# Optimization experiments

Measured on AMD Instinct MI355X. Metric: run time of the kernel, lower is better.

Reference implementation:

```python
import jax, jax.numpy as jnp
import numpy as np

N = 100000
E = 1600000
IN_C, HID, HEADS, OUT_C = 128, 32, 4, 32
NEG_SLOPE = 0.2


def gat_layer(x, edge_index, W, att_src, att_dst, bias, concat):
    """PyG-style GATConv: h = xW, per-edge attention, segment softmax over dst, scatter-add."""
    n = x.shape[0]
    H, C = att_src.shape
    h = (x @ W).reshape(n, H, C)                      # [N, H, C]
    src, dst = edge_index[0], edge_index[1]
    a_s = jnp.sum(h * att_src, axis=-1)               # [N, H]
    a_d = jnp.sum(h * att_dst, axis=-1)               # [N, H]
    e = jax.nn.leaky_relu(a_s[src] + a_d[dst], NEG_SLOPE)   # [E, H]
    # numerically stable segment softmax over incoming edges of each dst node
    m = jax.ops.segment_max(e, dst, num_segments=n)   # [N, H]
    ex = jnp.exp(e - m[dst])
    denom = jax.ops.segment_sum(ex, dst, num_segments=n)
    alpha = ex / denom[dst]                           # [E, H]
    msg = h[src] * alpha[:, :, None]                  # [E, H, C]
    out = jax.ops.segment_sum(msg, dst, num_segments=n)  # [N, H, C]
    out = out.reshape(n, H * C) if concat else out.mean(axis=1)
    return out + bias


def add_self_loops(edge_index, n):
    ar = jnp.arange(n, dtype=edge_index.dtype)
    loops = jnp.stack([ar, ar])
    return jnp.concatenate([edge_index, loops], axis=1)


def setup_inputs() -> dict:
    key = jax.random.key(0)
    ks = jax.random.split(key, 10)
    x = jax.random.normal(ks[0], (N, IN_C), dtype=jnp.float32)
    edge_index = jax.random.randint(ks[1], (2, E), 0, N, dtype=jnp.int64)
    s = 0.1
    W1 = jax.random.normal(ks[2], (IN_C, HEADS * HID), dtype=jnp.float32) * s
    att_src1 = jax.random.normal(ks[3], (HEADS, HID), dtype=jnp.float32) * s
    att_dst1 = jax.random.normal(ks[4], (HEADS, HID), dtype=jnp.float32) * s
    b1 = jnp.zeros((HEADS * HID,), dtype=jnp.float32)
    W2 = jax.random.normal(ks[5], (HEADS * HID, OUT_C), dtype=jnp.float32) * s
    att_src2 = jax.random.normal(ks[6], (1, OUT_C), dtype=jnp.float32) * s
    att_dst2 = jax.random.normal(ks[7], (1, OUT_C), dtype=jnp.float32) * s
    b2 = jnp.zeros((OUT_C,), dtype=jnp.float32)
    return {"x": x, "edge_index": edge_index,
            "W1": W1, "att_src1": att_src1, "att_dst1": att_dst1, "b1": b1,
            "W2": W2, "att_src2": att_src2, "att_dst2": att_dst2, "b2": b2}


def reference(x, edge_index, W1, att_src1, att_dst1, b1, W2, att_src2, att_dst2, b2):
    ei = add_self_loops(edge_index, x.shape[0])
    h = gat_layer(x, ei, W1, att_src1, att_dst1, b1, concat=True)
    h = jax.nn.elu(h)
    h = gat_layer(h, ei, W2, att_src2, att_dst2, b2, concat=False)
    return jax.nn.log_softmax(h, axis=1)
```

## Files before the change

### kernel.cpp

```cpp
#include <hip/hip_runtime.h>
#include <hip/hip_fp16.h>
#include <math.h>

#define IN_C   128
#define HEADS  4
#define F1     128
#define OUT_C  32
#define NEG    0.2f
#define SH     8
#define CHA    8192
#define SCB    4096

__device__ __forceinline__ unsigned short f2h(float f) {
    return __half_as_ushort(__float2half_rn(f));
}
__device__ __forceinline__ float h2f(unsigned short u) {
    return __half2float(__ushort_as_half(u));
}
__device__ __forceinline__ float hlo(unsigned u) { return h2f((unsigned short)(u & 0xffffu)); }
__device__ __forceinline__ float hhi(unsigned u) { return h2f((unsigned short)(u >> 16)); }
__device__ __forceinline__ unsigned pk2(float a, float b) {
    return (unsigned)f2h(a) | ((unsigned)f2h(b) << 16);
}
typedef _Float16 h2v __attribute__((ext_vector_type(2)));
__device__ __forceinline__ h2v u2h2(unsigned u) {
    h2v r; __builtin_memcpy(&r, &u, 4); return r;
}
__device__ __forceinline__ float dot2(unsigned a, unsigned b, float c) {
    return __builtin_amdgcn_fdot2(u2h2(a), u2h2(b), c, false);
}
#define PERM_LO 0x05040100u
#define PERM_HI 0x07060302u
__device__ __forceinline__ float pdot(unsigned b, unsigned a, unsigned sel, h2v pv, float c) {
    return __builtin_amdgcn_fdot2(u2h2(__builtin_amdgcn_perm(b, a, sel)), pv, c, false);
}

__global__ __launch_bounds__(256) void k_bhist(
    const int* __restrict__ ei, int* __restrict__ bmat, int E_, int n, int NB, int NC)
{
    __shared__ int h[512];
    int t = threadIdx.x, c = blockIdx.x;
    for (int i = t; i < NB; i += 256) h[i] = 0;
    __syncthreads();
    int e0 = c * CHA, e1 = min(e0 + CHA, E_ + n);
    for (int e = e0 + t; e < e1; e += 256) {
        int d = (e < E_) ? ei[E_ + e] : e - E_;
        atomicAdd(&h[d >> SH], 1);
    }
    __syncthreads();
    for (int i = t; i < NB; i += 256) bmat[i * NC + c] = h[i];
}

__global__ __launch_bounds__(256) void k_scanA(
    int* __restrict__ bmat, int* __restrict__ bsums, int M)
{
    __shared__ int sm[256];
    int t = threadIdx.x;
    int base = blockIdx.x * SCB + t * 16;
    int v[16];
    int s = 0;
    #pragma unroll
    for (int j = 0; j < 16; ++j) {
        int i = base + j;
        v[j] = (i < M) ? bmat[i] : 0;
        s += v[j];
    }
    sm[t] = s;
    __syncthreads();
    for (int off = 1; off < 256; off <<= 1) {
        int a = (t >= off) ? sm[t - off] : 0;
        __syncthreads();
        sm[t] += a;
        __syncthreads();
    }
    int excl = sm[t] - s;
    #pragma unroll
    for (int j = 0; j < 16; ++j) {
        int i = base + j;
        if (i < M) bmat[i] = excl;
        excl += v[j];
    }
    if (t == 255) bsums[blockIdx.x] = sm[255];
}

__global__ __launch_bounds__(256) void k_scanB(int* __restrict__ bsums, int NBLK)
{
    __shared__ int sm[256];
    int t = threadIdx.x;
    int v = (t < NBLK) ? bsums[t] : 0;
    sm[t] = v;
    __syncthreads();
    for (int off = 1; off < 256; off <<= 1) {
        int a = (t >= off) ? sm[t - off] : 0;
        __syncthreads();
        sm[t] += a;
        __syncthreads();
    }
    if (t < NBLK) bsums[t] = sm[t] - v;
}

__global__ __launch_bounds__(256) void k_scanC(
    int* __restrict__ bmat, const int* __restrict__ bsums, int M)
{
    int i = blockIdx.x * 256 + threadIdx.x;
    if (i < M) bmat[i] += bsums[i >> 12];
}

__global__ __launch_bounds__(256) void k_bscatter(
    const int* __restrict__ ei, const int* __restrict__ bmat,
    unsigned* __restrict__ recs, int E_, int n, int NB, int NC)
{
    __shared__ int cur[512];
    int t = threadIdx.x, c = blockIdx.x;
    for (int i = t; i < NB; i += 256) cur[i] = bmat[i * NC + c];
    __syncthreads();
    int e0 = c * CHA, e1 = min(e0 + CHA, E_ + n);
    for (int e = e0 + t; e < e1; e += 256) {
        int s, d;
        if (e < E_) { s = ei[e]; d = ei[E_ + e]; } else { s = d = e - E_; }
        int b = d >> SH;
        int p = atomicAdd(&cur[b], 1);
        recs[p] = ((unsigned)(d & ((1 << SH) - 1)) << 17) | (unsigned)s;
    }
}

__global__ __launch_bounds__(256) void k_bfill(
    const unsigned* __restrict__ recs, const int* __restrict__ bmat,
    int* __restrict__ row_off, int* __restrict__ csr, int n, int NB, int NC, int EE)
{
    __shared__ int deg[256];
    __shared__ int cur[256];
    int t = threadIdx.x, b = blockIdx.x;
    int r0 = bmat[b * NC];
    int r1 = (b + 1 < NB) ? bmat[(b + 1) * NC] : EE;
    deg[t] = 0;
    __syncthreads();
    for (int i = r0 + t; i < r1; i += 256)
        atomicAdd(&deg[recs[i] >> 17], 1);
    __syncthreads();
    int v = deg[t];
    for (int off = 1; off < 256; off <<= 1) {
        int a = (t >= off) ? deg[t - off] : 0;
        __syncthreads();
        deg[t] += a;
        __syncthreads();
    }
    int excl = deg[t] - v;
    int dst = (b << SH) + t;
    if (dst < n) row_off[dst] = r0 + excl;
    cur[t] = excl;
    if (b == NB - 1 && t == 0) row_off[n] = EE;
    __syncthreads();
    for (int i = r0 + t; i < r1; i += 256) {
        unsigned rec = recs[i];
        int dl = rec >> 17;
        int p = atomicAdd(&cur[dl], 1);
        csr[r0 + p] = (int)(rec & 0x1FFFFu);
    }
}

__global__ __launch_bounds__(256) void k_gemm1(
    const float* __restrict__ x, const float* __restrict__ W,
    const float* __restrict__ as_w, const float* __restrict__ ad_w,
    unsigned short* __restrict__ h1h, float* __restrict__ as1,
    float* __restrict__ ad1, int n)
{
    __shared__ unsigned Ws2[64 * 64];
    __shared__ unsigned xs2[64 * 64];
    int t = threadIdx.x;
    int half = blockIdx.x & 1;
    int n0 = (blockIdx.x >> 1) * 64;

    for (int i = t; i < 64 * 16; i += 256) {
        int k2 = i >> 4, c4 = (i & 15) * 4;
        const float* w0 = &W[(2 * k2) * 128 + half * 64 + c4];
        const float* w1 = &W[(2 * k2 + 1) * 128 + half * 64 + c4];
        float4 a = *(const float4*)w0;
        float4 b = *(const float4*)w1;
        uint4 p;
        p.x = pk2(a.x, b.x); p.y = pk2(a.y, b.y);
        p.z = pk2(a.z, b.z); p.w = pk2(a.w, b.w);
        *(uint4*)&Ws2[k2 * 64 + c4] = p;
    }
    for (int i = t; i < 64 * 32; i += 256) {
        int nl = i & 63, k4 = (i >> 6) * 4;
        int nn = n0 + nl;
        float4 v = (nn < n) ? *(const float4*)&x[(size_t)nn * 128 + k4]
                            : make_float4(0.f, 0.f, 0.f, 0.f);
        xs2[(k4 >> 1) * 64 + nl]       = pk2(v.x, v.y);
        xs2[((k4 >> 1) + 1) * 64 + nl] = pk2(v.z, v.w);
    }
    __syncthreads();

    int tx = t & 15, ty = t >> 4;
    float acc[4][4] = {};
    #pragma unroll 4
    for (int k2 = 0; k2 < 64; ++k2) {
        uint4 a = *(uint4*)&xs2[k2 * 64 + ty * 4];
        uint4 b = *(uint4*)&Ws2[k2 * 64 + tx * 4];
        unsigned av[4] = {a.x, a.y, a.z, a.w};
        unsigned bv[4] = {b.x, b.y, b.z, b.w};
        #pragma unroll
        for (int i = 0; i < 4; ++i)
            #pragma unroll
            for (int j = 0; j < 4; ++j)
                acc[i][j] = dot2(av[i], bv[j], acc[i][j]);
    }
    int cbase = half * 64 + tx * 4;
    float4 aws = *(const float4*)&as_w[cbase];
    float4 awd = *(const float4*)&ad_w[cbase];
    float sa[4], sd[4];
    #pragma unroll
    for (int i = 0; i < 4; ++i) {
        int nn = n0 + ty * 4 + i;
        sa[i] = acc[i][0]*aws.x + acc[i][1]*aws.y + acc[i][2]*aws.z + acc[i][3]*aws.w;
        sd[i] = acc[i][0]*awd.x + acc[i][1]*awd.y + acc[i][2]*awd.z + acc[i][3]*awd.w;
        if (nn < n) {
            ushort4 p;
            p.x = f2h(acc[i][0]); p.y = f2h(acc[i][1]);
            p.z = f2h(acc[i][2]); p.w = f2h(acc[i][3]);
            *(ushort4*)&h1h[(size_t)nn * 128 + cbase] = p;
        }
    }
    #pragma unroll
    for (int o = 1; o < 8; o <<= 1) {
        #pragma unroll
        for (int i = 0; i < 4; ++i) {
            sa[i] += __shfl_xor(sa[i], o);
            sd[i] += __shfl_xor(sd[i], o);
        }
    }
    if ((tx & 7) == 0) {
        int head = half * 2 + (tx >> 3);
        #pragma unroll
        for (int i = 0; i < 4; ++i) {
            int nn = n0 + ty * 4 + i;
            if (nn < n) {
                as1[(size_t)nn * 4 + head] = sa[i];
                ad1[(size_t)nn * 4 + head] = sd[i];
            }
        }
    }
}

__global__ __launch_bounds__(256) void k_gemm2(
    const float* __restrict__ z, const float* __restrict__ W,
    const float* __restrict__ as_w, const float* __restrict__ ad_w,
    unsigned short* __restrict__ h2h, float* __restrict__ as2,
    float* __restrict__ ad2, int n)
{
    __shared__ unsigned Ws2[64 * 32];
    __shared__ unsigned zs2[64 * 64];
    int t = threadIdx.x;
    int n0 = blockIdx.x * 64;

    for (int i = t; i < 64 * 8; i += 256) {
        int k2 = i >> 3, c4 = (i & 7) * 4;
        float4 a = *(const float4*)&W[(2 * k2) * 32 + c4];
        float4 b = *(const float4*)&W[(2 * k2 + 1) * 32 + c4];
        uint4 p;
        p.x = pk2(a.x, b.x); p.y = pk2(a.y, b.y);
        p.z = pk2(a.z, b.z); p.w = pk2(a.w, b.w);
        *(uint4*)&Ws2[k2 * 32 + c4] = p;
    }
    for (int i = t; i < 64 * 32; i += 256) {
        int nl = i & 63, k4 = (i >> 6) * 4;
        int nn = n0 + nl;
        float4 v = (nn < n) ? *(const float4*)&z[(size_t)nn * 128 + k4]
                            : make_float4(0.f, 0.f, 0.f, 0.f);
        zs2[(k4 >> 1) * 64 + nl]       = pk2(v.x, v.y);
        zs2[((k4 >> 1) + 1) * 64 + nl] = pk2(v.z, v.w);
    }
    __syncthreads();

    int tx = t & 7, ty = t >> 3;
    float acc[2][4] = {};
    #pragma unroll 4
    for (int k2 = 0; k2 < 64; ++k2) {
        uint2 a = *(uint2*)&zs2[k2 * 64 + ty * 2];
        uint4 b = *(uint4*)&Ws2[k2 * 32 + tx * 4];
        unsigned av[2] = {a.x, a.y};
        unsigned bv[4] = {b.x, b.y, b.z, b.w};
        #pragma unroll
        for (int i = 0; i < 2; ++i)
            #pragma unroll
            for (int j = 0; j < 4; ++j)
                acc[i][j] = dot2(av[i], bv[j], acc[i][j]);
    }
    float4 aws = *(const float4*)&as_w[tx * 4];
    float4 awd = *(const float4*)&ad_w[tx * 4];
    float sa[2], sd[2];
    #pragma unroll
    for (int i = 0; i < 2; ++i) {
        int nn = n0 + ty * 2 + i;
        sa[i] = acc[i][0]*aws.x + acc[i][1]*aws.y + acc[i][2]*aws.z + acc[i][3]*aws.w;
        sd[i] = acc[i][0]*awd.x + acc[i][1]*awd.y + acc[i][2]*awd.z + acc[i][3]*awd.w;
        if (nn < n) {
            ushort4 p;
            p.x = f2h(acc[i][0]); p.y = f2h(acc[i][1]);
            p.z = f2h(acc[i][2]); p.w = f2h(acc[i][3]);
            *(ushort4*)&h2h[(size_t)nn * 32 + tx * 4] = p;
        }
    }
    #pragma unroll
    for (int o = 1; o < 8; o <<= 1) {
        #pragma unroll
        for (int i = 0; i < 2; ++i) {
            sa[i] += __shfl_xor(sa[i], o);
            sd[i] += __shfl_xor(sd[i], o);
        }
    }
    if (tx == 0) {
        #pragma unroll
        for (int i = 0; i < 2; ++i) {
            int nn = n0 + ty * 2 + i;
            if (nn < n) { as2[nn] = sa[i]; ad2[nn] = sd[i]; }
        }
    }
}

__global__ __launch_bounds__(256) void k_gat1(
    const int* __restrict__ row_off, const int* __restrict__ csr,
    const float* __restrict__ as1, const float* __restrict__ ad1,
    const unsigned short* __restrict__ h1h, const float* __restrict__ b1,
    float* __restrict__ z, int n)
{
    int nb = threadIdx.x >> 4;
    int hl = threadIdx.x & 15;
    int node = blockIdx.x * 16 + nb;
    if (node >= n) return;
    __shared__ int            s_src[16][16];
    __shared__ unsigned short s_p16[16][4][16];
    int* ssrc = s_src[nb];
    unsigned short (*sp16)[16] = s_p16[nb];

    const char* h1b = (const char*)h1h;
    int chb  = hl << 4;
    int head = hl >> 2;

    float4 addv = *(const float4*)&ad1[(size_t)node * 4];
    int beg = row_off[node], end = row_off[node + 1];

    float sr0 = 0.f, sr1 = 0.f, sr2 = 0.f, sr3 = 0.f;
    float acc0 = 0.f, acc1 = 0.f, acc2 = 0.f, acc3 = 0.f;
    float acc4 = 0.f, acc5 = 0.f, acc6 = 0.f, acc7 = 0.f;

    for (int c = beg; c < end; c += 16) {
        int cnt = min(16, end - c);
        bool has = hl < cnt;
        float ls0 = 0.f, ls1 = 0.f, ls2 = 0.f, ls3 = 0.f;
        if (has) {
            int sA = csr[c + hl];
            ssrc[hl] = sA << 8;
            float4 av = *(const float4*)(as1 + ((unsigned)sA << 2));
            float v;
            v = av.x + addv.x; v = v > 0.f ? v : NEG * v; v = fminf(v, 10.f);
            unsigned short q0 = f2h(__expf(v));
            v = av.y + addv.y; v = v > 0.f ? v : NEG * v; v = fminf(v, 10.f);
            unsigned short q1 = f2h(__expf(v));
            v = av.z + addv.z; v = v > 0.f ? v : NEG * v; v = fminf(v, 10.f);
            unsigned short q2 = f2h(__expf(v));
            v = av.w + addv.w; v = v > 0.f ? v : NEG * v; v = fminf(v, 10.f);
            unsigned short q3 = f2h(__expf(v));
            sp16[0][hl] = q0; sp16[1][hl] = q1;
            sp16[2][hl] = q2; sp16[3][hl] = q3;
            ls0 = h2f(q0); ls1 = h2f(q1); ls2 = h2f(q2); ls3 = h2f(q3);
        }
        #pragma unroll
        for (int o = 8; o; o >>= 1) {
            ls0 += __shfl_xor(ls0, o);
            ls1 += __shfl_xor(ls1, o);
            ls2 += __shfl_xor(ls2, o);
            ls3 += __shfl_xor(ls3, o);
        }
        sr0 += ls0; sr1 += ls1; sr2 += ls2; sr3 += ls3;
        __threadfence_block();

        #define PAIR1(j) {                                                    \
            int2 oo = *(const int2*)&ssrc[j];                                 \
            unsigned pp = *(const unsigned*)&sp16[head][j];                   \
            uint4 A = *(const uint4*)(h1b + (unsigned)(oo.x + chb));          \
            uint4 B = *(const uint4*)(h1b + (unsigned)(oo.y + chb));          \
            h2v pv = u2h2(pp);                                                \
            acc0 = pdot(B.x, A.x, PERM_LO, pv, acc0);                         \
            acc1 = pdot(B.x, A.x, PERM_HI, pv, acc1);                         \
            acc2 = pdot(B.y, A.y, PERM_LO, pv, acc2);                         \
            acc3 = pdot(B.y, A.y, PERM_HI, pv, acc3);                         \
            acc4 = pdot(B.z, A.z, PERM_LO, pv, acc4);                         \
            acc5 = pdot(B.z, A.z, PERM_HI, pv, acc5);                         \
            acc6 = pdot(B.w, A.w, PERM_LO, pv, acc6);                         \
            acc7 = pdot(B.w, A.w, PERM_HI, pv, acc7);                         \
        }
        int jj = 0;
        for (; jj + 4 <= cnt; jj += 4) {
            PAIR1(jj);
            PAIR1(jj + 2);
        }
        if (jj + 2 <= cnt) {
            PAIR1(jj);
            jj += 2;
        }
        if (jj < cnt) {
            int o0 = ssrc[jj];
            float p = h2f(sp16[head][jj]);
            uint4 A = *(const uint4*)(h1b + (unsigned)(o0 + chb));
            acc0 = fmaf(p, hlo(A.x), acc0);
            acc1 = fmaf(p, hhi(A.x), acc1);
            acc2 = fmaf(p, hlo(A.y), acc2);
            acc3 = fmaf(p, hhi(A.y), acc3);
            acc4 = fmaf(p, hlo(A.z), acc4);
            acc5 = fmaf(p, hhi(A.z), acc5);
            acc6 = fmaf(p, hlo(A.w), acc6);
            acc7 = fmaf(p, hhi(A.w), acc7);
        }
        #undef PAIR1
    }
    float srh = head == 0 ? sr0 : head == 1 ? sr1 : head == 2 ? sr2 : sr3;
    float inv = 1.0f / srh;
    float4 bb0 = *(const float4*)&b1[hl * 8];
    float4 bb1 = *(const float4*)&b1[hl * 8 + 4];
    float v0 = acc0 * inv + bb0.x;
    float v1 = acc1 * inv + bb0.y;
    float v2 = acc2 * inv + bb0.z;
    float v3 = acc3 * inv + bb0.w;
    float v4 = acc4 * inv + bb1.x;
    float v5 = acc5 * inv + bb1.y;
    float v6 = acc6 * inv + bb1.z;
    float v7 = acc7 * inv + bb1.w;
    v0 = v0 > 0.f ? v0 : (__expf(v0) - 1.f);
    v1 = v1 > 0.f ? v1 : (__expf(v1) - 1.f);
    v2 = v2 > 0.f ? v2 : (__expf(v2) - 1.f);
    v3 = v3 > 0.f ? v3 : (__expf(v3) - 1.f);
    v4 = v4 > 0.f ? v4 : (__expf(v4) - 1.f);
    v5 = v5 > 0.f ? v5 : (__expf(v5) - 1.f);
    v6 = v6 > 0.f ? v6 : (__expf(v6) - 1.f);
    v7 = v7 > 0.f ? v7 : (__expf(v7) - 1.f);
    float* zr = &z[(size_t)node * F1 + hl * 8];
    *(float4*)zr       = make_float4(v0, v1, v2, v3);
    *(float4*)(zr + 4) = make_float4(v4, v5, v6, v7);
}

__global__ __launch_bounds__(256) void k_gat2(
    const int* __restrict__ row_off, const int* __restrict__ csr,
    const float* __restrict__ as2, const float* __restrict__ ad2,
    const unsigned short* __restrict__ h2h, const float* __restrict__ b2,
    float* __restrict__ y, int n)
{
    int nb = threadIdx.x >> 4;
    int hl = threadIdx.x & 15;
    int node = blockIdx.x * 16 + nb;
    if (node >= n) return;
    __shared__ int            s_src[16][16];
    __shared__ unsigned short s_p16[16][16];
    int* ssrc = s_src[nb];
    unsigned short* sp16 = s_p16[nb];

    const char* h2b = (const char*)h2h;
    int chb = hl << 2;

    float addv = ad2[node];
    int beg = row_off[node], end = row_off[node + 1];
    float sr = 0.f, acc0 = 0.f, acc1 = 0.f;

    for (int c = beg; c < end; c += 16) {
        int cnt = min(16, end - c);
        bool has = hl < cnt;
        float ls = 0.f;
        if (has) {
            int sA = csr[c + hl];
            ssrc[hl] = sA << 6;
            float v = as2[(unsigned)sA] + addv;
            v = v > 0.f ? v : NEG * v;
            v = fminf(v, 10.f);
            unsigned short q = f2h(__expf(v));
            sp16[hl] = q;
            ls = h2f(q);
        }
        #pragma unroll
        for (int o = 8; o; o >>= 1) ls += __shfl_xor(ls, o);
        sr += ls;
        __threadfence_block();

        #define PAIR2(j) {                                                    \
            int2 oo = *(const int2*)&ssrc[j];                                 \
            unsigned pp = *(const unsigned*)&sp16[j];                         \
            unsigned ua = *(const unsigned*)(h2b + (unsigned)(oo.x + chb));   \
            unsigned ub = *(const unsigned*)(h2b + (unsigned)(oo.y + chb));   \
            h2v pv = u2h2(pp);                                                \
            acc0 = pdot(ub, ua, PERM_LO, pv, acc0);                           \
            acc1 = pdot(ub, ua, PERM_HI, pv, acc1);                           \
        }
        int jj = 0;
        for (; jj + 4 <= cnt; jj += 4) {
            PAIR2(jj);
            PAIR2(jj + 2);
        }
        if (jj + 2 <= cnt) {
            PAIR2(jj);
            jj += 2;
        }
        if (jj < cnt) {
            unsigned ua = *(const unsigned*)(h2b + (unsigned)(ssrc[jj] + chb));
            float p = h2f(sp16[jj]);
            acc0 = fmaf(p, hlo(ua), acc0);
            acc1 = fmaf(p, hhi(ua), acc1);
        }
        #undef PAIR2
    }
    float inv = 1.0f / sr;
    float2 bb = *(const float2*)&b2[hl * 2];
    float v0 = acc0 * inv + bb.x;
    float v1 = acc1 * inv + bb.y;
    float m = fmaxf(v0, v1);
    #pragma unroll
    for (int o = 8; o; o >>= 1) m = fmaxf(m, __shfl_xor(m, o));
    float ss = __expf(v0 - m) + __expf(v1 - m);
    #pragma unroll
    for (int o = 8; o; o >>= 1) ss += __shfl_xor(ss, o);
    float lg = m + logf(ss);
    *(float2*)&y[(size_t)node * OUT_C + hl * 2] = make_float2(v0 - lg, v1 - lg);
}

extern "C" void kernel_launch(void* const* d_in, const int* in_sizes, int n_in,
                              void* d_out, int out_size, void* d_ws, size_t ws_size,
                              hipStream_t stream) {
    const float* x    = (const float*)d_in[0];
    const int*   ei   = (const int*)d_in[1];
    const float* W1   = (const float*)d_in[2];
    const float* as1w = (const float*)d_in[3];
    const float* ad1w = (const float*)d_in[4];
    const float* b1   = (const float*)d_in[5];
    const float* W2   = (const float*)d_in[6];
    const float* as2w = (const float*)d_in[7];
    const float* ad2w = (const float*)d_in[8];
    const float* b2   = (const float*)d_in[9];
    float* out = (float*)d_out;

    int n  = in_sizes[0] / IN_C;
    int E_ = in_sizes[1] / 2;
    int EE = E_ + n;

    int NB = (n + (1 << SH) - 1) >> SH;
    int NC = (EE + CHA - 1) / CHA;
    int M  = NB * NC;
    int NBLK = (M + SCB - 1) / SCB;

    char* w = (char*)d_ws;
    size_t off = 0;
    auto take = [&](size_t elems) { void* p = w + off; off += ((elems * 4 + 255) & ~(size_t)255); return p; };
    int* bmat      = (int*)take((size_t)M);
    int* bsums     = (int*)take(256);
    unsigned* recs = (unsigned*)take((size_t)EE);
    int* row_off   = (int*)take((size_t)n + 1);
    int* csr       = (int*)take((size_t)EE);
    float* as1     = (float*)take((size_t)n * 4);
    float* ad1     = (float*)take((size_t)n * 4);
    unsigned short* h1h = (unsigned short*)take((size_t)n * 64);
    float* z       = (float*)take((size_t)n * 128);
    unsigned short* h2h = (unsigned short*)take((size_t)n * 16);
    float* as2     = (float*)take((size_t)n);
    float* ad2     = (float*)take((size_t)n);

    k_bhist   <<<NC, 256, 0, stream>>>(ei, bmat, E_, n, NB, NC);
    k_scanA   <<<NBLK, 256, 0, stream>>>(bmat, bsums, M);
    k_scanB   <<<1, 256, 0, stream>>>(bsums, NBLK);
    k_scanC   <<<(M + 255) / 256, 256, 0, stream>>>(bmat, bsums, M);
    k_bscatter<<<NC, 256, 0, stream>>>(ei, bmat, recs, E_, n, NB, NC);
    k_bfill   <<<NB, 256, 0, stream>>>(recs, bmat, row_off, csr, n, NB, NC, EE);

    int nt = (n + 63) / 64;
    k_gemm1<<<nt * 2, 256, 0, stream>>>(x, W1, as1w, ad1w, h1h, as1, ad1, n);
    int gG = (n + 15) / 16;
    k_gat1<<<gG, 256, 0, stream>>>(row_off, csr, as1, ad1, h1h, b1, z, n);

    k_gemm2<<<nt, 256, 0, stream>>>(z, W2, as2w, ad2w, h2h, as2, ad2, n);
    k_gat2<<<gG, 256, 0, stream>>>(row_off, csr, as2, ad2, h2h, b2, out, n);
}
```

Measured before the change: 332.0 us.

## Sort nodes by in-degree for load-balanced GAT aggregation, widen edge chunks to 32

Builds a degree histogram during CSR construction, scans it, and scatters node ids into a degree-bucketed permutation. Both GAT aggregation kernels then process nodes in that order, so the 16-lane groups inside a block handle nodes of similar degree and diverge less. The softmax-weight stage now handles 32 edges per chunk with each lane computing two edges, which halves the outer loop trips for typical degrees. The cost is two extra small kernels and scattered output writes, because nodes are no longer processed in index order.

Result: slower. 611.0 us (+84.0%).

```diff
diff --git a/kernel.cpp b/kernel.cpp
--- a/kernel.cpp
+++ b/kernel.cpp
@@ -108,10 +108,11 @@
 
 __global__ __launch_bounds__(256) void k_bscatter(
     const int* __restrict__ ei, const int* __restrict__ bmat,
-    unsigned* __restrict__ recs, int E_, int n, int NB, int NC)
+    unsigned* __restrict__ recs, int* __restrict__ dhist, int E_, int n, int NB, int NC)
 {
     __shared__ int cur[512];
     int t = threadIdx.x, c = blockIdx.x;
+    if (c == 0 && t < 256) dhist[t] = 0;
     for (int i = t; i < NB; i += 256) cur[i] = bmat[i * NC + c];
     __syncthreads();
     int e0 = c * CHA, e1 = min(e0 + CHA, E_ + n);
@@ -126,7 +127,8 @@
 
 __global__ __launch_bounds__(256) void k_bfill(
     const unsigned* __restrict__ recs, const int* __restrict__ bmat,
-    int* __restrict__ row_off, int* __restrict__ csr, int n, int NB, int NC, int EE)
+    int* __restrict__ row_off, int* __restrict__ csr, int* __restrict__ dhist,
+    int n, int NB, int NC, int EE)
 {
     __shared__ int deg[256];
     __shared__ int cur[256];
@@ -147,7 +149,10 @@
     }
     int excl = deg[t] - v;
     int dst = (b << SH) + t;
-    if (dst < n) row_off[dst] = r0 + excl;
+    if (dst < n) {
+        row_off[dst] = r0 + excl;
+        atomicAdd(&dhist[min(v, 255)], 1);
+    }
     cur[t] = excl;
     if (b == NB - 1 && t == 0) row_off[n] = EE;
     __syncthreads();
@@ -157,6 +162,28 @@
         int p = atomicAdd(&cur[dl], 1);
         csr[r0 + p] = (int)(rec & 0x1FFFFu);
     }
+}
+
+__global__ __launch_bounds__(256) void k_pscatter(
+    const int* __restrict__ row_off, int* __restrict__ cur,
+    int* __restrict__ perm, int n)
+{
+    __shared__ int bh[256], bbase[256];
+    int t = threadIdx.x;
+    int i = blockIdx.x * 256 + t;
+    bh[t] = 0;
+    __syncthreads();
+    int bin = 0, rk = 0;
+    bool val = i < n;
+    if (val) {
+        int deg = row_off[i + 1] - row_off[i];
+        bin = min(deg, 255);
+        rk = atomicAdd(&bh[bin], 1);
+    }
+    __syncthreads();
+    if (bh[t] > 0) bbase[t] = atomicAdd(&cur[t], bh[t]);
+    __syncthreads();
+    if (val) perm[bbase[bin] + rk] = i;
 }
 
 __global__ __launch_bounds__(256) void k_gemm1(
@@ -320,6 +347,7 @@
 }
 
 __global__ __launch_bounds__(256) void k_gat1(
+    const int* __restrict__ perm,
     const int* __restrict__ row_off, const int* __restrict__ csr,
     const float* __restrict__ as1, const float* __restrict__ ad1,
     const unsigned short* __restrict__ h1h, const float* __restrict__ b1,
@@ -327,12 +355,13 @@
 {
     int nb = threadIdx.x >> 4;
     int hl = threadIdx.x & 15;
-    int node = blockIdx.x * 16 + nb;
-    if (node >= n) return;
-    __shared__ int            s_src[16][16];
-    __shared__ unsigned short s_p16[16][4][16];
+    int r = blockIdx.x * 16 + nb;
+    if (r >= n) return;
+    int node = perm[r];
+    __shared__ int            s_src[16][32];
+    __shared__ unsigned short s_p16[16][4][32];
     int* ssrc = s_src[nb];
-    unsigned short (*sp16)[16] = s_p16[nb];
+    unsigned short (*sp16)[32] = s_p16[nb];
 
     const char* h1b = (const char*)h1h;
     int chb  = hl << 4;
@@ -345,26 +374,38 @@
     float acc0 = 0.f, acc1 = 0.f, acc2 = 0.f, acc3 = 0.f;
     float acc4 = 0.f, acc5 = 0.f, acc6 = 0.f, acc7 = 0.f;
 
-    for (int c = beg; c < end; c += 16) {
-        int cnt = min(16, end - c);
-        bool has = hl < cnt;
+    for (int c = beg; c < end; c += 32) {
+        int cnt = min(32, end - c);
+        int e0 = hl << 1;
         float ls0 = 0.f, ls1 = 0.f, ls2 = 0.f, ls3 = 0.f;
-        if (has) {
-            int sA = csr[c + hl];
-            ssrc[hl] = sA << 8;
-            float4 av = *(const float4*)(as1 + ((unsigned)sA << 2));
+        if (e0 < cnt) {
+            int sA = csr[c + e0];
+            ssrc[e0] = sA << 8;
+            float4 avA = *(const float4*)(as1 + ((unsigned)sA << 2));
             float v;
-            v = av.x + addv.x; v = v > 0.f ? v : NEG * v; v = fminf(v, 10.f);
-            unsigned short q0 = f2h(__expf(v));
-            v = av.y + addv.y; v = v > 0.f ? v : NEG * v; v = fminf(v, 10.f);
-            unsigned short q1 = f2h(__expf(v));
-            v = av.z + addv.z; v = v > 0.f ? v : NEG * v; v = fminf(v, 10.f);
-            unsigned short q2 = f2h(__expf(v));
-            v = av.w + addv.w; v = v > 0.f ? v : NEG * v; v = fminf(v, 10.f);
-            unsigned short q3 = f2h(__expf(v));
-            sp16[0][hl] = q0; sp16[1][hl] = q1;
-            sp16[2][hl] = q2; sp16[3][hl] = q3;
-            ls0 = h2f(q0); ls1 = h2f(q1); ls2 = h2f(q2); ls3 = h2f(q3);
+            unsigned short qa0, qa1, qa2, qa3;
+            unsigned short qb0 = 0, qb1 = 0, qb2 = 0, qb3 = 0;
+            v = avA.x + addv.x; v = v > 0.f ? v : NEG * v; qa0 = f2h(__expf(fminf(v, 10.f)));
+            v = avA.y + addv.y; v = v > 0.f ? v : NEG * v; qa1 = f2h(__expf(fminf(v, 10.f)));
+            v = avA.z + addv.z; v = v > 0.f ? v : NEG * v; qa2 = f2h(__expf(fminf(v, 10.f)));
+            v = avA.w + addv.w; v = v > 0.f ? v : NEG * v; qa3 = f2h(__expf(fminf(v, 10.f)));
+            if (e0 + 1 < cnt) {
+                int sB = csr[c + e0 + 1];
+                ssrc[e0 + 1] = sB << 8;
+                float4 avB = *(const float4*)(as1 + ((unsigned)sB << 2));
+                v = avB.x + addv.x; v = v > 0.f ? v : NEG * v; qb0 = f2h(__expf(fminf(v, 10.f)));
+                v = avB.y + addv.y; v = v > 0.f ? v : NEG * v; qb1 = f2h(__expf(fminf(v, 10.f)));
+                v = avB.z + addv.z; v = v > 0.f ? v : NEG * v; qb2 = f2h(__expf(fminf(v, 10.f)));
+                v = avB.w + addv.w; v = v > 0.f ? v : NEG * v; qb3 = f2h(__expf(fminf(v, 10.f)));
+            }
+            *(unsigned*)&sp16[0][e0] = (unsigned)qa0 | ((unsigned)qb0 << 16);
+            *(unsigned*)&sp16[1][e0] = (unsigned)qa1 | ((unsigned)qb1 << 16);
+            *(unsigned*)&sp16[2][e0] = (unsigned)qa2 | ((unsigned)qb2 << 16);
+            *(unsigned*)&sp16[3][e0] = (unsigned)qa3 | ((unsigned)qb3 << 16);
+            ls0 = h2f(qa0) + h2f(qb0);
+            ls1 = h2f(qa1) + h2f(qb1);
+            ls2 = h2f(qa2) + h2f(qb2);
+            ls3 = h2f(qa3) + h2f(qb3);
         }
         #pragma unroll
         for (int o = 8; o; o >>= 1) {
@@ -441,6 +482,7 @@
 }
 
 __global__ __launch_bounds__(256) void k_gat2(
+    const int* __restrict__ perm,
     const int* __restrict__ row_off, const int* __restrict__ csr,
     const float* __restrict__ as2, const float* __restrict__ ad2,
     const unsigned short* __restrict__ h2h, const float* __restrict__ b2,
@@ -448,10 +490,11 @@
 {
     int nb = threadIdx.x >> 4;
     int hl = threadIdx.x & 15;
-    int node = blockIdx.x * 16 + nb;
-    if (node >= n) return;
-    __shared__ int            s_src[16][16];
-    __shared__ unsigned short s_p16[16][16];
+    int r = blockIdx.x * 16 + nb;
+    if (r >= n) return;
+    int node = perm[r];
+    __shared__ int            s_src[16][32];
+    __shared__ unsigned short s_p16[16][32];
     int* ssrc = s_src[nb];
     unsigned short* sp16 = s_p16[nb];
 
@@ -462,19 +505,26 @@
     int beg = row_off[node], end = row_off[node + 1];
     float sr = 0.f, acc0 = 0.f, acc1 = 0.f;
 
-    for (int c = beg; c < end; c += 16) {
-        int cnt = min(16, end - c);
-        bool has = hl < cnt;
+    for (int c = beg; c < end; c += 32) {
+        int cnt = min(32, end - c);
+        int e0 = hl << 1;
         float ls = 0.f;
-        if (has) {
-            int sA = csr[c + hl];
-            ssrc[hl] = sA << 6;
+        if (e0 < cnt) {
+            int sA = csr[c + e0];
+            ssrc[e0] = sA << 6;
             float v = as2[(unsigned)sA] + addv;
             v = v > 0.f ? v : NEG * v;
-            v = fminf(v, 10.f);
-            unsigned short q = f2h(__expf(v));
-            sp16[hl] = q;
-            ls = h2f(q);
+            unsigned short qa = f2h(__expf(fminf(v, 10.f)));
+            unsigned short qb = 0;
+            if (e0 + 1 < cnt) {
+                int sB = csr[c + e0 + 1];
+                ssrc[e0 + 1] = sB << 6;
+                float w = as2[(unsigned)sB] + addv;
+                w = w > 0.f ? w : NEG * w;
+                qb = f2h(__expf(fminf(w, 10.f)));
+            }
+            *(unsigned*)&sp16[e0] = (unsigned)qa | ((unsigned)qb << 16);
+            ls = h2f(qa) + h2f(qb);
         }
         #pragma unroll
         for (int o = 8; o; o >>= 1) ls += __shfl_xor(ls, o);
@@ -561,18 +611,24 @@
     float* as2     = (float*)take((size_t)n);
     float* ad2     = (float*)take((size_t)n);
 
+    int* dhist = bsums;
+    int* perm  = (int*)recs;
+
     k_bhist   <<<NC, 256, 0, stream>>>(ei, bmat, E_, n, NB, NC);
     k_scanA   <<<NBLK, 256, 0, stream>>>(bmat, bsums, M);
     k_scanB   <<<1, 256, 0, stream>>>(bsums, NBLK);
     k_scanC   <<<(M + 255) / 256, 256, 0, stream>>>(bmat, bsums, M);
-    k_bscatter<<<NC, 256, 0, stream>>>(ei, bmat, recs, E_, n, NB, NC);
-    k_bfill   <<<NB, 256, 0, stream>>>(recs, bmat, row_off, csr, n, NB, NC, EE);
+    k_bscatter<<<NC, 256, 0, stream>>>(ei, bmat, recs, dhist, E_, n, NB, NC);
+    k_bfill   <<<NB, 256, 0, stream>>>(recs, bmat, row_off, csr, dhist, n, NB, NC, EE);
+
+    k_scanB   <<<1, 256, 0, stream>>>(dhist, 256);
+    k_pscatter<<<(n + 255) / 256, 256, 0, stream>>>(row_off, dhist, perm, n);
 
     int nt = (n + 63) / 64;
     k_gemm1<<<nt * 2, 256, 0, stream>>>(x, W1, as1w, ad1w, h1h, as1, ad1, n);
     int gG = (n + 15) / 16;
-    k_gat1<<<gG, 256, 0, stream>>>(row_off, csr, as1, ad1, h1h, b1, z, n);
+    k_gat1<<<gG, 256, 0, stream>>>(perm, row_off, csr, as1, ad1, h1h, b1, z, n);
 
     k_gemm2<<<nt, 256, 0, stream>>>(z, W2, as2w, ad2w, h2h, as2, ad2, n);
-    k_gat2<<<gG, 256, 0, stream>>>(row_off, csr, as2, ad2, h2h, b2, out, n);
-}
+    k_gat2<<<gG, 256, 0, stream>>>(perm, row_off, csr, as2, ad2, h2h, b2, out, n);
+}
```

## Remap layer-2 aggregation to 4 lanes per node with 16-byte gathers

Applied to the files above, without the earlier changes.

The second GAT aggregation kernel now assigns 4 threads per destination node (64 nodes per block) instead of 16. Each lane gathers 16 bytes (8 fp16 channels) per source edge and keeps 8 accumulators, and edge chunks grow to 32 so each lane computes 8 attention weights. This cuts the number of small gather instructions and shuffle steps, and raises the number of nodes per wave so low-degree nodes waste fewer lanes. In exchange it adds register pressure and serializes more per-edge exp work onto each lane.

Measured after the change: 339.3 us. +2.2%, slower.

```diff
diff --git a/kernel.cpp b/kernel.cpp
--- a/kernel.cpp
+++ b/kernel.cpp
@@ -446,49 +446,68 @@
     const unsigned short* __restrict__ h2h, const float* __restrict__ b2,
     float* __restrict__ y, int n)
 {
-    int nb = threadIdx.x >> 4;
-    int hl = threadIdx.x & 15;
-    int node = blockIdx.x * 16 + nb;
+    int nb = threadIdx.x >> 2;
+    int hl = threadIdx.x & 3;
+    int node = blockIdx.x * 64 + nb;
     if (node >= n) return;
-    __shared__ int            s_src[16][16];
-    __shared__ unsigned short s_p16[16][16];
+    __shared__ int            s_src[64][34];
+    __shared__ unsigned short s_p16[64][34];
     int* ssrc = s_src[nb];
     unsigned short* sp16 = s_p16[nb];
 
     const char* h2b = (const char*)h2h;
-    int chb = hl << 2;
+    int chb = hl << 4;
 
     float addv = ad2[node];
     int beg = row_off[node], end = row_off[node + 1];
-    float sr = 0.f, acc0 = 0.f, acc1 = 0.f;
-
-    for (int c = beg; c < end; c += 16) {
-        int cnt = min(16, end - c);
-        bool has = hl < cnt;
+    float sr = 0.f;
+    float acc0 = 0.f, acc1 = 0.f, acc2 = 0.f, acc3 = 0.f;
+    float acc4 = 0.f, acc5 = 0.f, acc6 = 0.f, acc7 = 0.f;
+
+    for (int c = beg; c < end; c += 32) {
+        int cnt = min(32, end - c);
+        int e0 = hl << 3;
         float ls = 0.f;
-        if (has) {
-            int sA = csr[c + hl];
-            ssrc[hl] = sA << 6;
-            float v = as2[(unsigned)sA] + addv;
-            v = v > 0.f ? v : NEG * v;
-            v = fminf(v, 10.f);
-            unsigned short q = f2h(__expf(v));
-            sp16[hl] = q;
-            ls = h2f(q);
-        }
-        #pragma unroll
-        for (int o = 8; o; o >>= 1) ls += __shfl_xor(ls, o);
+        #pragma unroll
+        for (int k = 0; k < 8; k += 2) {
+            int e = e0 + k;
+            if (e < cnt) {
+                unsigned short qa, qb = 0;
+                int sA = csr[c + e];
+                ssrc[e] = sA << 6;
+                float v = as2[(unsigned)sA] + addv;
+                v = v > 0.f ? v : NEG * v;
+                qa = f2h(__expf(fminf(v, 10.f)));
+                if (e + 1 < cnt) {
+                    int sB = csr[c + e + 1];
+                    ssrc[e + 1] = sB << 6;
+                    float w2 = as2[(unsigned)sB] + addv;
+                    w2 = w2 > 0.f ? w2 : NEG * w2;
+                    qb = f2h(__expf(fminf(w2, 10.f)));
+                }
+                *(unsigned*)&sp16[e] = (unsigned)qa | ((unsigned)qb << 16);
+                ls += h2f(qa) + h2f(qb);
+            }
+        }
+        ls += __shfl_xor(ls, 1);
+        ls += __shfl_xor(ls, 2);
         sr += ls;
         __threadfence_block();
 
         #define PAIR2(j) {                                                    \
             int2 oo = *(const int2*)&ssrc[j];                                 \
             unsigned pp = *(const unsigned*)&sp16[j];                         \
-            unsigned ua = *(const unsigned*)(h2b + (unsigned)(oo.x + chb));   \
-            unsigned ub = *(const unsigned*)(h2b + (unsigned)(oo.y + chb));   \
+            uint4 A = *(const uint4*)(h2b + (unsigned)(oo.x + chb));          \
+            uint4 B = *(const uint4*)(h2b + (unsigned)(oo.y + chb));          \
             h2v pv = u2h2(pp);                                                \
-            acc0 = pdot(ub, ua, PERM_LO, pv, acc0);                           \
-            acc1 = pdot(ub, ua, PERM_HI, pv, acc1);                           \
+            acc0 = pdot(B.x, A.x, PERM_LO, pv, acc0);                         \
+            acc1 = pdot(B.x, A.x, PERM_HI, pv, acc1);                         \
+            acc2 = pdot(B.y, A.y, PERM_LO, pv, acc2);                         \
+            acc3 = pdot(B.y, A.y, PERM_HI, pv, acc3);                         \
+            acc4 = pdot(B.z, A.z, PERM_LO, pv, acc4);                         \
+            acc5 = pdot(B.z, A.z, PERM_HI, pv, acc5);                         \
+            acc6 = pdot(B.w, A.w, PERM_LO, pv, acc6);                         \
+            acc7 = pdot(B.w, A.w, PERM_HI, pv, acc7);                         \
         }
         int jj = 0;
         for (; jj + 4 <= cnt; jj += 4) {
@@ -500,25 +519,43 @@
             jj += 2;
         }
         if (jj < cnt) {
-            unsigned ua = *(const unsigned*)(h2b + (unsigned)(ssrc[jj] + chb));
+            int o0 = ssrc[jj];
             float p = h2f(sp16[jj]);
-            acc0 = fmaf(p, hlo(ua), acc0);
-            acc1 = fmaf(p, hhi(ua), acc1);
+            uint4 A = *(const uint4*)(h2b + (unsigned)(o0 + chb));
+            acc0 = fmaf(p, hlo(A.x), acc0);
+            acc1 = fmaf(p, hhi(A.x), acc1);
+            acc2 = fmaf(p, hlo(A.y), acc2);
+            acc3 = fmaf(p, hhi(A.y), acc3);
+            acc4 = fmaf(p, hlo(A.z), acc4);
+            acc5 = fmaf(p, hhi(A.z), acc5);
+            acc6 = fmaf(p, hlo(A.w), acc6);
+            acc7 = fmaf(p, hhi(A.w), acc7);
         }
         #undef PAIR2
     }
     float inv = 1.0f / sr;
-    float2 bb = *(const float2*)&b2[hl * 2];
-    float v0 = acc0 * inv + bb.x;
-    float v1 = acc1 * inv + bb.y;
-    float m = fmaxf(v0, v1);
-    #pragma unroll
-    for (int o = 8; o; o >>= 1) m = fmaxf(m, __shfl_xor(m, o));
-    float ss = __expf(v0 - m) + __expf(v1 - m);
-    #pragma unroll
-    for (int o = 8; o; o >>= 1) ss += __shfl_xor(ss, o);
+    float4 bb0 = *(const float4*)&b2[hl * 8];
+    float4 bb1 = *(const float4*)&b2[hl * 8 + 4];
+    float v0 = acc0 * inv + bb0.x;
+    float v1 = acc1 * inv + bb0.y;
+    float v2 = acc2 * inv + bb0.z;
+    float v3 = acc3 * inv + bb0.w;
+    float v4 = acc4 * inv + bb1.x;
+    float v5 = acc5 * inv + bb1.y;
+    float v6 = acc6 * inv + bb1.z;
+    float v7 = acc7 * inv + bb1.w;
+    float m = fmaxf(fmaxf(fmaxf(v0, v1), fmaxf(v2, v3)),
+                    fmaxf(fmaxf(v4, v5), fmaxf(v6, v7)));
+    m = fmaxf(m, __shfl_xor(m, 1));
+    m = fmaxf(m, __shfl_xor(m, 2));
+    float ss = __expf(v0 - m) + __expf(v1 - m) + __expf(v2 - m) + __expf(v3 - m)
+             + __expf(v4 - m) + __expf(v5 - m) + __expf(v6 - m) + __expf(v7 - m);
+    ss += __shfl_xor(ss, 1);
+    ss += __shfl_xor(ss, 2);
     float lg = m + logf(ss);
-    *(float2*)&y[(size_t)node * OUT_C + hl * 2] = make_float2(v0 - lg, v1 - lg);
+    float* yr = &y[(size_t)node * OUT_C + hl * 8];
+    *(float4*)yr       = make_float4(v0 - lg, v1 - lg, v2 - lg, v3 - lg);
+    *(float4*)(yr + 4) = make_float4(v4 - lg, v5 - lg, v6 - lg, v7 - lg);
 }
 
 extern "C" void kernel_launch(void* const* d_in, const int* in_sizes, int n_in,
@@ -574,5 +611,6 @@
     k_gat1<<<gG, 256, 0, stream>>>(row_off, csr, as1, ad1, h1h, b1, z, n);
 
     k_gemm2<<<nt, 256, 0, stream>>>(z, W2, as2w, ad2w, h2h, as2, ad2, n);
-    k_gat2<<<gG, 256, 0, stream>>>(row_off, csr, as2, ad2, h2h, b2, out, n);
-}
+    int gG2 = (n + 63) / 64;
+    k_gat2<<<gG2, 256, 0, stream>>>(row_off, csr, as2, ad2, h2h, b2, out, n);
+}
```
